# Kernel tuning notes

Hardware: AMD Instinct MI355X
Metric: run time of the kernel (lower is better)

Reference implementation:

```python
import jax, jax.numpy as jnp
import numpy as np


def setup_inputs() -> dict:
    key = jax.random.key(0)
    ks = jax.random.split(key, 7)
    B, T, DIN, D = 64, 512, 512, 512
    s_in = 1.0 / np.sqrt(DIN)  # ~glorot-ish scale for input kernels
    s_h = 1.0 / np.sqrt(D)     # scale for recurrent kernels (orthogonal-ish magnitude)
    return {
        "X": jax.random.normal(ks[0], (B, T, DIN), jnp.float32),
        "W_z": jax.random.normal(ks[1], (DIN, D), jnp.float32) * s_in,
        "U_z": jax.random.normal(ks[2], (D, D), jnp.float32) * s_h,
        "b_z": jnp.zeros((D,), jnp.float32),
        "W_r": jax.random.normal(ks[3], (DIN, D), jnp.float32) * s_in,
        "U_r": jax.random.normal(ks[4], (D, D), jnp.float32) * s_h,
        "b_r": jnp.zeros((D,), jnp.float32),
        "W_h": jax.random.normal(ks[5], (DIN, D), jnp.float32) * s_in,
        "U_h": jax.random.normal(ks[6], (D, D), jnp.float32) * s_h,
        "b_h": jnp.zeros((D,), jnp.float32),
        "mask": jnp.ones((B, T), jnp.int32),
    }


def reference(X, W_z, U_z, b_z, W_r, U_r, b_r, W_h, U_h, b_h, mask):
    # X: [B, T, DIN] -> time-major [T, B, DIN]
    Xt = jnp.transpose(X, (1, 0, 2))
    # Precompute input projections (large GEMMs, done once): [T, B, D]
    xz = Xt @ W_z + b_z
    xr = Xt @ W_r + b_r
    xh = Xt @ W_h + b_h
    # Padded/shifted mask (pad=1): step t sees mask[t-1]; step 0 sees 0,
    # which zeroes the (zero) initial state exactly as in the theano code.
    m = jnp.transpose(mask, (1, 0)).astype(X.dtype)[:, :, None]  # [T, B, 1]
    m_tm1 = jnp.concatenate([jnp.zeros_like(m[:1]), m[:-1]], axis=0)

    B = X.shape[0]
    D = W_z.shape[1]
    h0 = jnp.zeros((B, D), X.dtype)

    def step(h_tm1, inputs):
        xz_t, xr_t, xh_t, mt = inputs
        hm = mt * h_tm1                                  # masked previous state
        z = jax.nn.sigmoid(xz_t + hm @ U_z)              # update gate
        r = jax.nn.sigmoid(xr_t + hm @ U_r)              # reset gate
        hh = jnp.tanh(xh_t + (r * hm) @ U_h)             # candidate
        h_t = z * hm + (1.0 - z) * hh
        return h_t, None

    h_last, _ = jax.lax.scan(step, h0, (xz, xr, xh, m_tm1))
    # return_sequences=False -> last hidden state [B, D]
    return h_last
```

## Files before the change

### kernel.cpp

```cpp
#include <hip/hip_runtime.h>
#include <hip/hip_fp16.h>

#define B_   64
#define T_   512
#define DINc 512
#define D_   512
#define NWG  16
#define JS   32

typedef _Float16 half8 __attribute__((ext_vector_type(8)));
typedef _Float16 half4 __attribute__((ext_vector_type(4)));
typedef float   floatx4 __attribute__((ext_vector_type(4)));
typedef unsigned uintx4 __attribute__((ext_vector_type(4)));

#define WAITV(N) asm volatile("s_waitcnt vmcnt(" #N ")" ::: "memory")
#define SCB()    __builtin_amdgcn_sched_barrier(0)

__global__ __launch_bounds__(256) void k_cvtX(const float* __restrict__ X, _Float16* __restrict__ Xh) {
    int idx = blockIdx.x * 256 + threadIdx.x;
    int m  = idx >> 6;
    int k8 = idx & 63;
    int b = m & 63, t = m >> 6;
    const float* src = X + ((size_t)(b * T_ + t)) * DINc + k8 * 8;
    float4 f0 = *(const float4*)(src);
    float4 f1 = *(const float4*)(src + 4);
    half8 h;
    h[0] = (_Float16)f0.x; h[1] = (_Float16)f0.y; h[2] = (_Float16)f0.z; h[3] = (_Float16)f0.w;
    h[4] = (_Float16)f1.x; h[5] = (_Float16)f1.y; h[6] = (_Float16)f1.z; h[7] = (_Float16)f1.w;
    *(half8*)(Xh + (size_t)m * DINc + k8 * 8) = h;
}

__global__ __launch_bounds__(256) void k_cvtW(const float* __restrict__ M0, const float* __restrict__ M1,
                                              const float* __restrict__ M2, _Float16* __restrict__ Mt) {
    __shared__ float tile[64][65];
    int g = blockIdx.z;
    const float* W = (g == 0) ? M0 : ((g == 1) ? M1 : M2);
    int n0 = blockIdx.x * 64, k0 = blockIdx.y * 64;
    int c = threadIdx.x & 63, r4 = threadIdx.x >> 6;
#pragma unroll
    for (int i = 0; i < 16; ++i) {
        int k = r4 + i * 4;
        tile[k][c] = W[(size_t)(k0 + k) * D_ + n0 + c];
    }
    __syncthreads();
    _Float16* out = Mt + (size_t)g * D_ * DINc;
#pragma unroll
    for (int i = 0; i < 16; ++i) {
        int n = r4 + i * 4;
        out[(size_t)(n0 + n) * DINc + k0 + c] = (_Float16)tile[c][n];
    }
}

__global__ __launch_bounds__(256) void k_cvtM(const int* __restrict__ mask, float* __restrict__ maskT) {
    int idx = blockIdx.x * 256 + threadIdx.x;
    int t = idx >> 6, b = idx & 63;
    maskT[idx] = (float)mask[(size_t)b * T_ + t];
}

__global__ __launch_bounds__(256) void k_gemm(const _Float16* __restrict__ Xh, const _Float16* __restrict__ Wt,
                                              const float* __restrict__ bz, const float* __restrict__ br,
                                              const float* __restrict__ bh, _Float16* __restrict__ xprojT) {
    __shared__ _Float16 As[128 * 32];
    __shared__ _Float16 Bs[128 * 32];
    int g = blockIdx.z;
    const _Float16* Wg = Wt + (size_t)g * 512 * 512;
    const float* bias = (g == 0) ? bz : ((g == 1) ? br : bh);
    _Float16* out = xprojT + (size_t)g * 16777216;
    int mb = blockIdx.x * 128, nb = blockIdx.y * 128;
    int tid = threadIdx.x, l = tid & 63, w = tid >> 6;
    int wr = w >> 1, wc = w & 1;
    int lr = l & 15, lg = l >> 4;

    floatx4 acc[4][4] = {};

    int ga0 = tid, ga1 = tid + 256;
    int ra0 = ga0 >> 2, ca0 = (ga0 & 3) * 8;
    int ra1 = ga1 >> 2, ca1 = (ga1 & 3) * 8;

    uint4 pa0, pa1, pb0, pb1;
    pa0 = *(const uint4*)(Xh + (size_t)(mb + ra0) * 512 + ca0);
    pa1 = *(const uint4*)(Xh + (size_t)(mb + ra1) * 512 + ca1);
    pb0 = *(const uint4*)(Wg + (size_t)(nb + ra0) * 512 + ca0);
    pb1 = *(const uint4*)(Wg + (size_t)(nb + ra1) * 512 + ca1);

    for (int kt = 0; kt < 16; ++kt) {
        __syncthreads();
        *(uint4*)(&As[ga0 * 8]) = pa0;
        *(uint4*)(&As[ga1 * 8]) = pa1;
        *(uint4*)(&Bs[ga0 * 8]) = pb0;
        *(uint4*)(&Bs[ga1 * 8]) = pb1;
        __syncthreads();
        if (kt < 15) {
            int kb = (kt + 1) * 32;
            pa0 = *(const uint4*)(Xh + (size_t)(mb + ra0) * 512 + kb + ca0);
            pa1 = *(const uint4*)(Xh + (size_t)(mb + ra1) * 512 + kb + ca1);
            pb0 = *(const uint4*)(Wg + (size_t)(nb + ra0) * 512 + kb + ca0);
            pb1 = *(const uint4*)(Wg + (size_t)(nb + ra1) * 512 + kb + ca1);
        }
        half8 af[4], bf[4];
#pragma unroll
        for (int mi = 0; mi < 4; mi++) af[mi] = *(const half8*)(&As[(wr * 64 + mi * 16 + lr) * 32 + lg * 8]);
#pragma unroll
        for (int ni = 0; ni < 4; ni++) bf[ni] = *(const half8*)(&Bs[(wc * 64 + ni * 16 + lr) * 32 + lg * 8]);
#pragma unroll
        for (int mi = 0; mi < 4; mi++)
#pragma unroll
            for (int ni = 0; ni < 4; ni++)
                acc[mi][ni] = __builtin_amdgcn_mfma_f32_16x16x32_f16(af[mi], bf[ni], acc[mi][ni], 0, 0, 0);
    }

#pragma unroll
    for (int ni = 0; ni < 4; ni++) {
        int col = nb + wc * 64 + ni * 16 + lr;
        float bv = bias[col];
#pragma unroll
        for (int mi = 0; mi < 4; mi++) {
            int row = mb + wr * 64 + mi * 16 + lg * 4;
            int tt = row >> 6, bb = row & 63;
            half4 hv;
#pragma unroll
            for (int i = 0; i < 4; i++) hv[i] = (_Float16)(acc[mi][ni][i] + bv);
            *(half4*)(out + (size_t)tt * 32768 + (size_t)col * 64 + bb) = hv;
        }
    }
}

__device__ __forceinline__ void st_agent(unsigned long long* p, unsigned long long v) {
    __hip_atomic_store(p, v, __ATOMIC_RELAXED, __HIP_MEMORY_SCOPE_AGENT);
}
__device__ __forceinline__ uintx4 ld16_agent(const void* p) {
    uintx4 r;
    asm volatile("global_load_dwordx4 %0, %1, off sc0 sc1" : "=v"(r) : "v"(p) : "memory");
    return r;
}
__device__ __forceinline__ bool chunk_valid(uintx4 v) {
    return ((v[0] & v[1]) != 0xFFFFFFFFu) && ((v[2] & v[3]) != 0xFFFFFFFFu);
}

__device__ __forceinline__ unsigned long long pack_quad(const float v4[4], int lr) {
    unsigned long long unit = 0;
    int j = lr & 3;
#pragma unroll
    for (int i = 0; i < 4; i++) {
        _Float16 hv = (_Float16)v4[i];
        unsigned int v = (unsigned int)__builtin_bit_cast(unsigned short, hv);
        unsigned int o1 = __shfl_xor(v, 1, 64);
        unsigned int pair = (lr & 1) ? (o1 | (v << 16)) : (v | (o1 << 16));
        unsigned int q2 = __shfl_xor(pair, 2, 64);
        unsigned long long u = (lr & 2) ? ((unsigned long long)q2 | ((unsigned long long)pair << 32))
                                        : ((unsigned long long)pair | ((unsigned long long)q2 << 32));
        if (i == j) unit = u;
    }
    return unit;
}

__global__ __launch_bounds__(512) void k_scan(const _Float16* __restrict__ Ut,
                                              const float* __restrict__ maskT,
                                              const _Float16* __restrict__ xprojT,
                                              unsigned long long* __restrict__ hbuf,
                                              unsigned long long* __restrict__ rhbuf,
                                              float* __restrict__ out) {
    __shared__ __align__(16) _Float16 Ulds[2 * JS * 512];
    __shared__ __align__(16) _Float16 Stg[64 * 512];
    char* StgB = (char*)Stg;
    int tid = threadIdx.x, l = tid & 63, w = tid >> 6;
    int lr = l & 15, lg = l >> 4;
    int mt = w >> 1, nt = w & 1;
    int slot = blockIdx.x;
    int jsb = slot * JS;

    for (int c = tid; c < 2 * JS * 64; c += 512) {
        int g  = c >> 11;
        int n  = (c >> 6) & 31;
        int k16 = c & 63;
        uintx4 v = *(const uintx4*)(Ut + (size_t)g * 262144 + (size_t)(jsb + n) * 512 + k16 * 8);
        *(uintx4*)((char*)Ulds + g * 32768 + n * 1024 + ((k16 * 16) ^ ((n & 7) << 4))) = v;
    }
    half8 uhf[16];
    {
        const _Float16* UtH = Ut + (size_t)2 * 262144;
        int ncol = jsb + nt * 16 + lr;
#pragma unroll
        for (int j = 0; j < 16; j++)
            uhf[j] = *(const half8*)(UtH + (size_t)ncol * 512 + j * 32 + lg * 8);
    }
    __syncthreads();

    const char* UB = (const char*)Ulds + (nt * 16 + lr) * 1024;
    const int swz = (lr & 7) << 4;

    int row0 = mt * 16 + lg * 4;
    int colg = jsb + nt * 16 + lr;

    float h4[4]  = {0.f, 0.f, 0.f, 0.f};
    float hm4[4] = {0.f, 0.f, 0.f, 0.f};

    const int punit = (mt * 16 + lg * 4 + (lr & 3)) * 128 + ((jsb + nt * 16) >> 2) + ((lr >> 2) & 3);
    const char* SB = StgB + (mt * 16 + lr) * 1024;

    const _Float16* xzB = xprojT + (size_t)colg * 64 + row0;
    const _Float16* xrB = xzB + (size_t)16777216;
    const _Float16* xhB = xrB + (size_t)16777216;

    {
        half4 xz0 = *(const half4*)(xzB);
        half4 xh0 = *(const half4*)(xhB);
        float4 m0 = *(const float4*)(maskT + row0);
#pragma unroll
        for (int i = 0; i < 4; i++) {
            float z  = __builtin_amdgcn_rcpf(1.f + __expf(-(float)xz0[i]));
            float hh = tanhf((float)xh0[i]);
            h4[i]  = (1.f - z) * hh;
            hm4[i] = ((float)m0[i]) * h4[i];
        }
        st_agent(hbuf + punit, pack_quad(hm4, lr));
    }

    for (int t = 1; t < T_; ++t) {
        const char* hmG = (const char*)(hbuf + ((t - 1) & 1) * 8192);
        unsigned long long* rhPsn = rhbuf + ((t - 1) & 1) * 8192;
        unsigned long long* hPsn  = hbuf  + ((t - 1) & 1) * 8192;
        unsigned long long* rhW   = rhbuf + (t & 1) * 8192;
        unsigned long long* hW    = hbuf  + (t & 1) * 8192;
        const char* rhG = (const char*)rhW;

        half4 xzp = *(const half4*)(xzB + (size_t)t * 32768);
        half4 xrp = *(const half4*)(xrB + (size_t)t * 32768);
        half4 xhp = *(const half4*)(xhB + (size_t)t * 32768);
        float4 mv = *(const float4*)(maskT + (size_t)t * 64 + row0);

        uintx4 gg[8];
        {
            unsigned vmask = 0;
#pragma unroll
            for (int it = 0; it < 8; ++it)
                gg[it] = ld16_agent(hmG + (w * 8 + it) * 1024 + l * 16);
            WAITV(0); SCB();
#pragma unroll
            for (int it = 0; it < 8; ++it) if (chunk_valid(gg[it])) vmask |= 1u << it;
            while (!__all(vmask == 255u)) {
#pragma unroll
                for (int it = 0; it < 8; ++it)
                    if (!(vmask & (1u << it)))
                        gg[it] = ld16_agent(hmG + (w * 8 + it) * 1024 + l * 16);
                WAITV(0); SCB();
#pragma unroll
                for (int it = 0; it < 8; ++it) if (chunk_valid(gg[it])) vmask |= 1u << it;
            }
        }
        st_agent(rhPsn + punit, ~0ull);
        __syncthreads();
#pragma unroll
        for (int it = 0; it < 8; ++it)
            *(uintx4*)(StgB + (w * 8 + it) * 1024 + ((l * 16) ^ (it << 4))) = gg[it];
        __syncthreads();
        half8 af[16];
#pragma unroll
        for (int j = 0; j < 16; j++)
            af[j] = *(const half8*)(SB + ((j * 64 + lg * 16) ^ swz));
        floatx4 accr = {0.f, 0.f, 0.f, 0.f};
        __builtin_amdgcn_s_setprio(1);
#pragma unroll
        for (int j = 0; j < 16; j++) {
            int boff = (j * 64 + lg * 16) ^ swz;
            half8 br8 = *(const half8*)(UB + 32768 + boff);
            accr = __builtin_amdgcn_mfma_f32_16x16x32_f16(af[j], br8, accr, 0, 0, 0);
        }
        __builtin_amdgcn_s_setprio(0);
        float rh4[4];
#pragma unroll
        for (int i = 0; i < 4; i++) {
            float rr = __builtin_amdgcn_rcpf(1.f + __expf(-((float)xrp[i] + accr[i])));
            rh4[i] = rr * hm4[i];
        }
        st_agent(rhW + punit, pack_quad(rh4, lr));
        floatx4 accz = {0.f, 0.f, 0.f, 0.f};
        __builtin_amdgcn_s_setprio(1);
#pragma unroll
        for (int j = 0; j < 16; j++) {
            int boff = (j * 64 + lg * 16) ^ swz;
            half8 bz8 = *(const half8*)(UB + boff);
            accz = __builtin_amdgcn_mfma_f32_16x16x32_f16(af[j], bz8, accz, 0, 0, 0);
        }
        __builtin_amdgcn_s_setprio(0);
        float z4[4];
#pragma unroll
        for (int i = 0; i < 4; i++)
            z4[i] = __builtin_amdgcn_rcpf(1.f + __expf(-((float)xzp[i] + accz[i])));

        uintx4 gg2[8];
        {
            unsigned vmask = 0;
#pragma unroll
            for (int it = 0; it < 8; ++it)
                gg2[it] = ld16_agent(rhG + (w * 8 + it) * 1024 + l * 16);
            WAITV(0); SCB();
#pragma unroll
            for (int it = 0; it < 8; ++it) if (chunk_valid(gg2[it])) vmask |= 1u << it;
            while (!__all(vmask == 255u)) {
#pragma unroll
                for (int it = 0; it < 8; ++it)
                    if (!(vmask & (1u << it)))
                        gg2[it] = ld16_agent(rhG + (w * 8 + it) * 1024 + l * 16);
                WAITV(0); SCB();
#pragma unroll
                for (int it = 0; it < 8; ++it) if (chunk_valid(gg2[it])) vmask |= 1u << it;
            }
        }
        st_agent(hPsn + punit, ~0ull);
        __syncthreads();
#pragma unroll
        for (int it = 0; it < 8; ++it)
            *(uintx4*)(StgB + (w * 8 + it) * 1024 + ((l * 16) ^ (it << 4))) = gg2[it];
        __syncthreads();
        half8 af2[16];
#pragma unroll
        for (int j = 0; j < 16; j++)
            af2[j] = *(const half8*)(SB + ((j * 64 + lg * 16) ^ swz));
        floatx4 acch0 = {0.f, 0.f, 0.f, 0.f}, acch1 = {0.f, 0.f, 0.f, 0.f};
        __builtin_amdgcn_s_setprio(1);
#pragma unroll
        for (int j = 0; j < 16; j += 2) {
            acch0 = __builtin_amdgcn_mfma_f32_16x16x32_f16(af2[j],     uhf[j],     acch0, 0, 0, 0);
            acch1 = __builtin_amdgcn_mfma_f32_16x16x32_f16(af2[j + 1], uhf[j + 1], acch1, 0, 0, 0);
        }
        __builtin_amdgcn_s_setprio(0);
#pragma unroll
        for (int i = 0; i < 4; i++) {
            float hh = tanhf((float)xhp[i] + acch0[i] + acch1[i]);
            h4[i]  = z4[i] * hm4[i] + (1.f - z4[i]) * hh;
            hm4[i] = ((float)mv[i]) * h4[i];
        }
        if (t < T_ - 1)
            st_agent(hW + punit, pack_quad(hm4, lr));
    }

#pragma unroll
    for (int i = 0; i < 4; i++)
        out[(size_t)(row0 + i) * 512 + colg] = h4[i];
}

extern "C" void kernel_launch(void* const* d_in, const int* in_sizes, int n_in,
                              void* d_out, int out_size, void* d_ws, size_t ws_size,
                              hipStream_t stream) {
    (void)in_sizes; (void)n_in; (void)out_size; (void)ws_size;
    const float* X  = (const float*)d_in[0];
    const float* Wz = (const float*)d_in[1];
    const float* Uz = (const float*)d_in[2];
    const float* bz = (const float*)d_in[3];
    const float* Wr = (const float*)d_in[4];
    const float* Ur = (const float*)d_in[5];
    const float* br = (const float*)d_in[6];
    const float* Wh = (const float*)d_in[7];
    const float* Uh = (const float*)d_in[8];
    const float* bh = (const float*)d_in[9];
    const int* mask = (const int*)d_in[10];
    float* out = (float*)d_out;

    char* ws = (char*)d_ws;
    unsigned long long* hbuf  = (unsigned long long*)(ws + 16384);
    unsigned long long* rhbuf = (unsigned long long*)(ws + 16384 + 131072);
    _Float16* Xh     = (_Float16*)(ws + 16384 + 2 * 131072);
    _Float16* Wt     = (_Float16*)(ws + 16384 + 2 * 131072 + 33554432);
    _Float16* Ut     = (_Float16*)(ws + 16384 + 2 * 131072 + 33554432 + 1572864);
    _Float16* xprojT = (_Float16*)(ws + 16384 + 2 * 131072 + 33554432 + 2 * 1572864);
    float*    maskT  = (float*)(ws + 16384 + 2 * 131072 + 33554432 + 2 * 1572864 + 100663296);

    hipMemsetAsync(ws + 16384, 0xFF, 2 * 131072, stream);
    hipLaunchKernelGGL(k_cvtX, dim3(8192), dim3(256), 0, stream, X, Xh);
    hipLaunchKernelGGL(k_cvtW, dim3(8, 8, 3), dim3(256), 0, stream, Wz, Wr, Wh, Wt);
    hipLaunchKernelGGL(k_cvtW, dim3(8, 8, 3), dim3(256), 0, stream, Uz, Ur, Uh, Ut);
    hipLaunchKernelGGL(k_cvtM, dim3(128), dim3(256), 0, stream, mask, maskT);
    hipLaunchKernelGGL(k_gemm, dim3(256, 4, 3), dim3(256), 0, stream, Xh, Wt, bz, br, bh, xprojT);
    hipLaunchKernelGGL(k_scan, dim3(NWG), dim3(512), 0, stream, Ut, maskT, xprojT,
                       hbuf, rhbuf, out);
}
```

Before: 4.256 ms.

## Add per-wave counter flags polled before poisoned-buffer data loads in GRU scan

Adds per-wave monotonic step counters (fh, fr) that each producing wave publishes after writing its h or r*h chunk. Consumers spin on these small flags before issuing the bulk poison-checked data loads, and a __syncthreads now precedes each poll. The intent is to cut the costly repeated 16-byte reloads of the large exchange buffers while waiting on other workgroups. It also drops the s_setprio boosts around the MFMA loops and now always writes the last h. The flags and data use only relaxed stores with no fences, so ordering between them is not guaranteed, and the extra syncs and flag round trip add latency on every step.

```diff
diff --git a/kernel.cpp b/kernel.cpp
--- a/kernel.cpp
+++ b/kernel.cpp
@@ -128,6 +128,12 @@
 __device__ __forceinline__ void st_agent(unsigned long long* p, unsigned long long v) {
     __hip_atomic_store(p, v, __ATOMIC_RELAXED, __HIP_MEMORY_SCOPE_AGENT);
 }
+__device__ __forceinline__ unsigned ld_flag(const unsigned* p) {
+    return __hip_atomic_load(p, __ATOMIC_RELAXED, __HIP_MEMORY_SCOPE_AGENT);
+}
+__device__ __forceinline__ void st_flag(unsigned* p, unsigned v) {
+    __hip_atomic_store(p, v, __ATOMIC_RELAXED, __HIP_MEMORY_SCOPE_AGENT);
+}
 __device__ __forceinline__ uintx4 ld16_agent(const void* p) {
     uintx4 r;
     asm volatile("global_load_dwordx4 %0, %1, off sc0 sc1" : "=v"(r) : "v"(p) : "memory");
@@ -154,11 +160,21 @@
     return unit;
 }
 
+__device__ __forceinline__ void poll_flags(const unsigned* f, unsigned need, int l) {
+    for (;;) {
+        unsigned v0 = ld_flag(f + l * 16);
+        unsigned v1 = ld_flag(f + (64 + l) * 16);
+        if (__all(v0 >= need && v1 >= need)) break;
+    }
+    SCB();
+}
+
 __global__ __launch_bounds__(512) void k_scan(const _Float16* __restrict__ Ut,
                                               const float* __restrict__ maskT,
                                               const _Float16* __restrict__ xprojT,
                                               unsigned long long* __restrict__ hbuf,
                                               unsigned long long* __restrict__ rhbuf,
+                                              unsigned* __restrict__ fh, unsigned* __restrict__ fr,
                                               float* __restrict__ out) {
     __shared__ __align__(16) _Float16 Ulds[2 * JS * 512];
     __shared__ __align__(16) _Float16 Stg[64 * 512];
@@ -168,6 +184,7 @@
     int mt = w >> 1, nt = w & 1;
     int slot = blockIdx.x;
     int jsb = slot * JS;
+    const int fidx = slot * 8 + w;
 
     for (int c = tid; c < 2 * JS * 64; c += 512) {
         int g  = c >> 11;
@@ -214,6 +231,7 @@
             hm4[i] = ((float)m0[i]) * h4[i];
         }
         st_agent(hbuf + punit, pack_quad(hm4, lr));
+        if (l == 0) st_flag(fh + fidx * 16, 1u);
     }
 
     for (int t = 1; t < T_; ++t) {
@@ -229,6 +247,8 @@
         half4 xhp = *(const half4*)(xhB + (size_t)t * 32768);
         float4 mv = *(const float4*)(maskT + (size_t)t * 64 + row0);
 
+        __syncthreads();
+        poll_flags(fh, (unsigned)t, l);
         uintx4 gg[8];
         {
             unsigned vmask = 0;
@@ -259,14 +279,12 @@
         for (int j = 0; j < 16; j++)
             af[j] = *(const half8*)(SB + ((j * 64 + lg * 16) ^ swz));
         floatx4 accr = {0.f, 0.f, 0.f, 0.f};
-        __builtin_amdgcn_s_setprio(1);
 #pragma unroll
         for (int j = 0; j < 16; j++) {
             int boff = (j * 64 + lg * 16) ^ swz;
             half8 br8 = *(const half8*)(UB + 32768 + boff);
             accr = __builtin_amdgcn_mfma_f32_16x16x32_f16(af[j], br8, accr, 0, 0, 0);
         }
-        __builtin_amdgcn_s_setprio(0);
         float rh4[4];
 #pragma unroll
         for (int i = 0; i < 4; i++) {
@@ -274,20 +292,21 @@
             rh4[i] = rr * hm4[i];
         }
         st_agent(rhW + punit, pack_quad(rh4, lr));
+        if (l == 0) st_flag(fr + fidx * 16, (unsigned)t);
         floatx4 accz = {0.f, 0.f, 0.f, 0.f};
-        __builtin_amdgcn_s_setprio(1);
 #pragma unroll
         for (int j = 0; j < 16; j++) {
             int boff = (j * 64 + lg * 16) ^ swz;
             half8 bz8 = *(const half8*)(UB + boff);
             accz = __builtin_amdgcn_mfma_f32_16x16x32_f16(af[j], bz8, accz, 0, 0, 0);
         }
-        __builtin_amdgcn_s_setprio(0);
         float z4[4];
 #pragma unroll
         for (int i = 0; i < 4; i++)
             z4[i] = __builtin_amdgcn_rcpf(1.f + __expf(-((float)xzp[i] + accz[i])));
 
+        __syncthreads();
+        poll_flags(fr, (unsigned)t, l);
         uintx4 gg2[8];
         {
             unsigned vmask = 0;
@@ -318,21 +337,19 @@
         for (int j = 0; j < 16; j++)
             af2[j] = *(const half8*)(SB + ((j * 64 + lg * 16) ^ swz));
         floatx4 acch0 = {0.f, 0.f, 0.f, 0.f}, acch1 = {0.f, 0.f, 0.f, 0.f};
-        __builtin_amdgcn_s_setprio(1);
 #pragma unroll
         for (int j = 0; j < 16; j += 2) {
             acch0 = __builtin_amdgcn_mfma_f32_16x16x32_f16(af2[j],     uhf[j],     acch0, 0, 0, 0);
             acch1 = __builtin_amdgcn_mfma_f32_16x16x32_f16(af2[j + 1], uhf[j + 1], acch1, 0, 0, 0);
         }
-        __builtin_amdgcn_s_setprio(0);
 #pragma unroll
         for (int i = 0; i < 4; i++) {
             float hh = tanhf((float)xhp[i] + acch0[i] + acch1[i]);
             h4[i]  = z4[i] * hm4[i] + (1.f - z4[i]) * hh;
             hm4[i] = ((float)mv[i]) * h4[i];
         }
-        if (t < T_ - 1)
-            st_agent(hW + punit, pack_quad(hm4, lr));
+        st_agent(hW + punit, pack_quad(hm4, lr));
+        if (l == 0) st_flag(fh + fidx * 16, (unsigned)(t + 1));
     }
 
 #pragma unroll
@@ -358,6 +375,8 @@
     float* out = (float*)d_out;
 
     char* ws = (char*)d_ws;
+    unsigned* fh = (unsigned*)ws;
+    unsigned* fr = (unsigned*)(ws + 8192);
     unsigned long long* hbuf  = (unsigned long long*)(ws + 16384);
     unsigned long long* rhbuf = (unsigned long long*)(ws + 16384 + 131072);
     _Float16* Xh     = (_Float16*)(ws + 16384 + 2 * 131072);
@@ -366,6 +385,7 @@
     _Float16* xprojT = (_Float16*)(ws + 16384 + 2 * 131072 + 33554432 + 2 * 1572864);
     float*    maskT  = (float*)(ws + 16384 + 2 * 131072 + 33554432 + 2 * 1572864 + 100663296);
 
+    hipMemsetAsync(ws, 0, 16384, stream);
     hipMemsetAsync(ws + 16384, 0xFF, 2 * 131072, stream);
     hipLaunchKernelGGL(k_cvtX, dim3(8192), dim3(256), 0, stream, X, Xh);
     hipLaunchKernelGGL(k_cvtW, dim3(8, 8, 3), dim3(256), 0, stream, Wz, Wr, Wh, Wt);
@@ -373,5 +393,5 @@
     hipLaunchKernelGGL(k_cvtM, dim3(128), dim3(256), 0, stream, mask, maskT);
     hipLaunchKernelGGL(k_gemm, dim3(256, 4, 3), dim3(256), 0, stream, Xh, Wt, bz, br, bh, xprojT);
     hipLaunchKernelGGL(k_scan, dim3(NWG), dim3(512), 0, stream, Ut, maskT, xprojT,
-                       hbuf, rhbuf, out);
-}
+                       hbuf, rhbuf, fh, fr, out);
+}
```

Result: faster. 3.947 ms (-7.3%).
